# Kernel tuning notes

Hardware: AMD Instinct MI355X
Metric: run time of the kernel (lower is better)

## Reference

```python
import jax, jax.numpy as jnp
import numpy as np

IN_CH = 256
MED_CH = IN_CH // 2


def setup_inputs() -> dict:
    key = jax.random.key(0)
    ks = jax.random.split(key, 9)
    B, C, H, W = 16, IN_CH, 64, 64
    s = 1.0 / np.sqrt(C)
    sm = 1.0 / np.sqrt(MED_CH)
    return {
        "x": jax.random.normal(ks[0], (B, C, H, W), dtype=jnp.float32),
        "w_o": jax.random.normal(ks[1], (MED_CH, C), dtype=jnp.float32) * s,
        "b_o": jax.random.normal(ks[2], (MED_CH,), dtype=jnp.float32) * 0.01,
        "w_v": jax.random.normal(ks[3], (MED_CH, C), dtype=jnp.float32) * s,
        "b_v": jax.random.normal(ks[4], (MED_CH,), dtype=jnp.float32) * 0.01,
        "w_c": jax.random.normal(ks[5], (C, MED_CH), dtype=jnp.float32) * sm,
        "b_c": jax.random.normal(ks[6], (C,), dtype=jnp.float32) * 0.01,
        "gamma": jax.random.normal(ks[7], (1,), dtype=jnp.float32) * 0.1,
    }


def reference(x, w_o, b_o, w_v, b_v, w_c, b_c, gamma):
    B, C, H, W = x.shape
    N = H * W
    xf = x.reshape(B, C, N)  # [B,C,N]
    # 1x1 convs == per-pixel linear projections
    o = jnp.einsum("mc,bcn->bmn", w_o, xf) + b_o[None, :, None]   # [B,M,N]
    v = jnp.einsum("mc,bcn->bmn", w_v, xf) + b_v[None, :, None]   # [B,M,N]
    x_o = o.transpose(0, 2, 1)                                     # [B,N,M]
    x_v = jax.nn.softmax(v, axis=-1)                               # softmax over N
    # NOTE: original code reuses conv_v for the 's' branch (conv_s unused)
    x_s = jax.nn.softmax(v.transpose(0, 2, 1), axis=-1)            # [B,N,M], softmax over M
    A = jnp.einsum("bmn,bnk->bmk", x_v, x_s)                       # [B,M,M]
    Bt = jnp.einsum("bnm,bmk->bnk", x_o, A).transpose(0, 2, 1)     # [B,M,N]
    out = jax.nn.relu(jnp.einsum("cm,bmn->bcn", w_c, Bt) + b_c[None, :, None])
    result = gamma[0] * out.reshape(B, C, H, W) + x
    return result
```

## Files before the change

### kernel.cpp

```cpp
#include <hip/hip_runtime.h>
#include <math.h>

constexpr int Bn = 16;
constexpr int Cn = 256;
constexpr int Mn = 128;
constexpr int Nn = 4096;

typedef short bf16x8 __attribute__((ext_vector_type(8)));
typedef float f32x4 __attribute__((ext_vector_type(4)));
typedef unsigned short us8 __attribute__((ext_vector_type(8)));
typedef unsigned short us4 __attribute__((ext_vector_type(4)));

static __device__ __forceinline__ unsigned short f2bf(float f) {
  union { float f; unsigned int u; } c{f};
  unsigned int u = c.u;
  u += 0x7FFFu + ((u >> 16) & 1u);
  return (unsigned short)(u >> 16);
}

__global__ __launch_bounds__(256) void k_prep_w(
    const float* __restrict__ w_o, const float* __restrict__ w_v,
    unsigned short* __restrict__ Wst, float* __restrict__ rs) {
  int idx = blockIdx.x * 256 + threadIdx.x;
  if (idx < Bn * Mn) rs[idx] = 0.f;
  int row = idx >> 6;
  int c4 = (idx & 63) * 4;
  const float* src = (row < Mn) ? &w_o[(size_t)row * Cn + c4]
                                : &w_v[(size_t)(row - Mn) * Cn + c4];
  float4 f = *(const float4*)src;
  us4 g = {f2bf(f.x), f2bf(f.y), f2bf(f.z), f2bf(f.w)};
  *(us4*)&Wst[(size_t)row * Cn + c4] = g;
}

__global__ __launch_bounds__(256) void k_prep_x(
    const float* __restrict__ x, unsigned short* __restrict__ xT) {
  const int b = blockIdx.z;
  const int c0 = blockIdx.y * 128;
  const int n0 = blockIdx.x * 64;
  const int t = threadIdx.x;
  const int n4 = (t & 15) * 4;
  const int c8 = c0 + (t >> 4) * 8;
  const float* xb = x + ((size_t)b * Cn + c8) * Nn + n0 + n4;
  float4 r[8];
#pragma unroll
  for (int i = 0; i < 8; ++i) r[i] = *(const float4*)&xb[(size_t)i * Nn];
  unsigned short* dst = xT + ((size_t)b * Nn + n0 + n4) * Cn + c8;
#pragma unroll
  for (int j = 0; j < 4; ++j) {
    us8 g;
#pragma unroll
    for (int i = 0; i < 8; ++i) g[i] = f2bf(((const float*)&r[i])[j]);
    *(us8*)&dst[(size_t)j * Cn] = g;
  }
}

__global__ __launch_bounds__(256) void k_proj_mfma(
    const unsigned short* __restrict__ Wst,
    const unsigned short* __restrict__ xT,
    const float* __restrict__ b_o, const float* __restrict__ b_v,
    unsigned short* __restrict__ oT, float* __restrict__ Ap,
    float* __restrict__ rs) {
  __shared__ us8 pool[16 * 128 * 2];
  __shared__ float cs_lds[4][128];
  unsigned short* ldsA = (unsigned short*)pool;
  unsigned short* ldsB = (unsigned short*)pool + 8 * 128 * 8;
  const int b = blockIdx.z;
  const int mt = blockIdx.y;
  const int nt = blockIdx.x;
  const int t = threadIdx.x;
  const int wave = t >> 6, lane = t & 63;
  const int quad = lane >> 4, l16 = lane & 15;
  const int wm = (wave & 1) * 64, wn = (wave >> 1) * 64;
  f32x4 acc[4][4] = {};
  const unsigned short* Wb = Wst + (size_t)mt * 128 * Cn;
  const unsigned short* xb = xT + ((size_t)b * Nn + nt * 128) * Cn;

  for (int k0 = 0; k0 < Cn; k0 += 64) {
#pragma unroll
    for (int p = 0; p < 4; ++p) {
      int s = p * 256 + t;
      int g = s >> 7, row = s & 127;
      *(uint4*)&ldsA[(size_t)s * 8] = *(const uint4*)&Wb[(size_t)row * Cn + k0 + g * 8];
      *(uint4*)&ldsB[(size_t)s * 8] = *(const uint4*)&xb[(size_t)row * Cn + k0 + g * 8];
    }
    __syncthreads();
#pragma unroll
    for (int s = 0; s < 2; ++s) {
      bf16x8 af[4], bfr[4];
#pragma unroll
      for (int i = 0; i < 4; ++i)
        af[i] = *(const bf16x8*)&ldsA[(size_t)((s * 4 + quad) * 128 + wm + i * 16 + l16) * 8];
#pragma unroll
      for (int j = 0; j < 4; ++j)
        bfr[j] = *(const bf16x8*)&ldsB[(size_t)((s * 4 + quad) * 128 + wn + j * 16 + l16) * 8];
      if (mt) {
#pragma unroll
        for (int i = 0; i < 4; ++i)
#pragma unroll
          for (int j = 0; j < 4; ++j)
            acc[i][j] = __builtin_amdgcn_mfma_f32_16x16x32_bf16(af[i], bfr[j], acc[i][j], 0, 0, 0);
      } else {
#pragma unroll
        for (int i = 0; i < 4; ++i)
#pragma unroll
          for (int j = 0; j < 4; ++j)
            acc[i][j] = __builtin_amdgcn_mfma_f32_16x16x32_bf16(bfr[i], af[j], acc[i][j], 0, 0, 0);
      }
    }
    __syncthreads();
  }

  if (!mt) {
    float bo_j[4];
#pragma unroll
    for (int j = 0; j < 4; ++j) bo_j[j] = b_o[wm + j * 16 + l16];
#pragma unroll
    for (int i = 0; i < 4; ++i) {
#pragma unroll
      for (int r = 0; r < 4; ++r) {
        int n = nt * 128 + wn + i * 16 + quad * 4 + r;
        unsigned short* row = &oT[((size_t)b * Nn + n) * Mn];
#pragma unroll
        for (int j = 0; j < 4; ++j)
          row[wm + j * 16 + l16] = f2bf(acc[i][j][r] + bo_j[j]);
      }
    }
    return;
  }

#pragma unroll
  for (int i = 0; i < 4; ++i) {
#pragma unroll
    for (int r = 0; r < 4; ++r) {
      float bi = b_v[wm + i * 16 + quad * 4 + r];
#pragma unroll
      for (int j = 0; j < 4; ++j)
        acc[i][j][r] = __expf(acc[i][j][r] + bi);
    }
  }

#pragma unroll
  for (int i = 0; i < 4; ++i) {
#pragma unroll
    for (int r = 0; r < 4; ++r) {
      float s = acc[i][0][r] + acc[i][1][r] + acc[i][2][r] + acc[i][3][r];
      s += __shfl_xor(s, 1); s += __shfl_xor(s, 2);
      s += __shfl_xor(s, 4); s += __shfl_xor(s, 8);
      if (l16 == 0)
        atomicAdd(&rs[b * Mn + wm + i * 16 + quad * 4 + r], s);
    }
  }

  float csj[4];
#pragma unroll
  for (int j = 0; j < 4; ++j) {
    float c = 0.f;
#pragma unroll
    for (int i = 0; i < 4; ++i)
#pragma unroll
      for (int r = 0; r < 4; ++r) c += acc[i][j][r];
    c += __shfl_xor(c, 16);
    c += __shfl_xor(c, 32);
    csj[j] = c;
  }
  if (quad == 0) {
#pragma unroll
    for (int j = 0; j < 4; ++j) cs_lds[wave][wn + j * 16 + l16] = csj[j];
  }
  __syncthreads();

  const int cbase = (wave >> 1) * 2;
  float rinv[4];
#pragma unroll
  for (int j = 0; j < 4; ++j) {
    int nl = wn + j * 16 + l16;
    rinv[j] = rsqrtf(cs_lds[cbase][nl] + cs_lds[cbase + 1][nl]);
  }

  unsigned short* Hs = (unsigned short*)pool;
  unsigned short* Ls = Hs + 16 * 128 * 8;
#pragma unroll
  for (int i = 0; i < 4; ++i) {
#pragma unroll
    for (int r = 0; r < 4; ++r) {
      int m = wm + i * 16 + quad * 4 + r;
#pragma unroll
      for (int j = 0; j < 4; ++j) {
        int nl = wn + j * 16 + l16;
        float u = acc[i][j][r] * rinv[j];
        unsigned short h = f2bf(u);
        union { unsigned int q; float f; } hf{(unsigned int)h << 16};
        int idx = ((nl >> 3) * 128 + (m ^ (nl >> 3))) * 8 + (nl & 7);
        Hs[idx] = h;
        Ls[idx] = f2bf(u - hf.f);
      }
    }
  }
  __syncthreads();

  const bf16x8* Hv = (const bf16x8*)pool;
  const bf16x8* Lv = Hv + 16 * 128;
#pragma unroll
  for (int i = 0; i < 4; ++i)
#pragma unroll
    for (int j = 0; j < 4; ++j) acc[i][j] = (f32x4){0.f, 0.f, 0.f, 0.f};
#pragma unroll
  for (int s = 0; s < 4; ++s) {
    int g = s * 4 + quad;
    bf16x8 hA[4], lA[4], hB[4], lB[4];
#pragma unroll
    for (int i = 0; i < 4; ++i) {
      int mi = wm + i * 16 + l16;
      int ki = wn + i * 16 + l16;
      hA[i] = Hv[g * 128 + (mi ^ g)];
      lA[i] = Lv[g * 128 + (mi ^ g)];
      hB[i] = Hv[g * 128 + (ki ^ g)];
      lB[i] = Lv[g * 128 + (ki ^ g)];
    }
#pragma unroll
    for (int i = 0; i < 4; ++i)
#pragma unroll
      for (int j = 0; j < 4; ++j) {
        acc[i][j] = __builtin_amdgcn_mfma_f32_16x16x32_bf16(hA[i], hB[j], acc[i][j], 0, 0, 0);
        acc[i][j] = __builtin_amdgcn_mfma_f32_16x16x32_bf16(hA[i], lB[j], acc[i][j], 0, 0, 0);
        acc[i][j] = __builtin_amdgcn_mfma_f32_16x16x32_bf16(lA[i], hB[j], acc[i][j], 0, 0, 0);
      }
  }

  float* Apb = Ap + ((size_t)nt * Bn + b) * (Mn * Mn);
#pragma unroll
  for (int i = 0; i < 4; ++i) {
#pragma unroll
    for (int r = 0; r < 4; ++r) {
      int m = wm + i * 16 + quad * 4 + r;
      float* row = &Apb[(size_t)m * Mn];
#pragma unroll
      for (int j = 0; j < 4; ++j)
        row[wn + j * 16 + l16] = acc[i][j][r];
    }
  }
}

__global__ __launch_bounds__(256) void k_reduceA(
    const float* __restrict__ Ap, const float* __restrict__ rs,
    float* __restrict__ A, int S) {
  int tid = blockIdx.x * 256 + threadIdx.x;
  int idx4 = tid * 4;
  int b = idx4 / (Mn * Mn);
  int off = idx4 - b * (Mn * Mn);
  float4 s = {0.f, 0.f, 0.f, 0.f};
  for (int s0 = 0; s0 < S; ++s0) {
    float4 p = *(const float4*)&Ap[((size_t)s0 * Bn + b) * (Mn * Mn) + off];
    s.x += p.x; s.y += p.y; s.z += p.z; s.w += p.w;
  }
  float sc = 1.0f / rs[b * Mn + (off >> 7)];
  s.x *= sc; s.y *= sc; s.z *= sc; s.w *= sc;
  *(float4*)&A[idx4] = s;
}

__global__ __launch_bounds__(256) void k_w2(
    const float* __restrict__ w_c, const float* __restrict__ A,
    unsigned short* __restrict__ W2bf) {
  __shared__ float As[64][68];
  __shared__ float wcs[64][68];
  const int b = blockIdx.z;
  const int m0 = blockIdx.x * 64;
  const int c0 = blockIdx.y * 64;
  const int t = threadIdx.x;
  const int tc = (t >> 4) * 4, tmm = (t & 15) * 4;
  float acc[4][4] = {};
  for (int k0 = 0; k0 < Mn; k0 += 64) {
    int r = t >> 2;
    int k4 = (t & 3) * 4;
#pragma unroll
    for (int p = 0; p < 4; ++p) {
      int k = k4 + p * 16;
      float4 a4 = *(const float4*)&A[((size_t)(b * Mn + m0 + r)) * Mn + k0 + k];
      As[k + 0][r] = a4.x; As[k + 1][r] = a4.y; As[k + 2][r] = a4.z; As[k + 3][r] = a4.w;
      float4 w4 = *(const float4*)&w_c[(size_t)(c0 + r) * Mn + k0 + k];
      wcs[k + 0][r] = w4.x; wcs[k + 1][r] = w4.y; wcs[k + 2][r] = w4.z; wcs[k + 3][r] = w4.w;
    }
    __syncthreads();
#pragma unroll
    for (int kk = 0; kk < 64; ++kk) {
      float4 w4 = *(const float4*)&wcs[kk][tc];
      float4 a4 = *(const float4*)&As[kk][tmm];
      float w[4] = {w4.x, w4.y, w4.z, w4.w};
      float a[4] = {a4.x, a4.y, a4.z, a4.w};
#pragma unroll
      for (int i = 0; i < 4; ++i)
#pragma unroll
        for (int jj = 0; jj < 4; ++jj) acc[i][jj] = fmaf(w[i], a[jj], acc[i][jj]);
    }
    __syncthreads();
  }
#pragma unroll
  for (int i = 0; i < 4; ++i) {
    us4 g4 = {f2bf(acc[i][0]), f2bf(acc[i][1]), f2bf(acc[i][2]), f2bf(acc[i][3])};
    *(us4*)&W2bf[((size_t)(b * Cn + c0 + tc + i)) * Mn + m0 + tmm] = g4;
  }
}

__global__ __launch_bounds__(256) void k_final_mfma(
    const unsigned short* __restrict__ W2bf, const unsigned short* __restrict__ oT,
    const float* __restrict__ x, const float* __restrict__ b_c,
    const float* __restrict__ gamma, float* __restrict__ out) {
  __shared__ us8 ldsA[128 * 16];
  __shared__ us8 ldsB[128 * 16];
  const int b = blockIdx.z;
  const int c_t = blockIdx.y * 128;
  const int n_t = blockIdx.x * 128;
  const int t = threadIdx.x;
  const int wave = t >> 6, lane = t & 63;
  const int quad = lane >> 4, l16 = lane & 15;
  const int wc = (wave & 1) * 64, wn = (wave >> 1) * 64;
  const unsigned short* W2b = W2bf + ((size_t)b * Cn + c_t) * Mn;
  const unsigned short* oTb = oT + ((size_t)b * Nn + n_t) * Mn;

#pragma unroll
  for (int p = 0; p < 8; ++p) {
    int s = p * 256 + t;
    int row = s >> 4, g = s & 15;
    int slot = row * 16 + (g ^ (row & 15));
    ldsA[slot] = *(const us8*)&W2b[(size_t)row * Mn + g * 8];
    ldsB[slot] = *(const us8*)&oTb[(size_t)row * Mn + g * 8];
  }
  __syncthreads();

  f32x4 acc[4][4] = {};
#pragma unroll
  for (int s = 0; s < 4; ++s) {
    int gq = s * 4 + quad;
    int xo = gq ^ l16;
    bf16x8 af[4], bfr[4];
#pragma unroll
    for (int i = 0; i < 4; ++i)
      af[i] = *(const bf16x8*)&ldsA[(wc + i * 16 + l16) * 16 + xo];
#pragma unroll
    for (int j = 0; j < 4; ++j)
      bfr[j] = *(const bf16x8*)&ldsB[(wn + j * 16 + l16) * 16 + xo];
#pragma unroll
    for (int i = 0; i < 4; ++i)
#pragma unroll
      for (int j = 0; j < 4; ++j)
        acc[i][j] = __builtin_amdgcn_mfma_f32_16x16x32_bf16(af[i], bfr[j], acc[i][j], 0, 0, 0);
  }

  float g = gamma[0];
#pragma unroll
  for (int i = 0; i < 4; ++i) {
#pragma unroll
    for (int r = 0; r < 4; ++r) {
      int c = c_t + wc + i * 16 + quad * 4 + r;
      float bias = b_c[c];
      const float* xr = &x[((size_t)b * Cn + c) * Nn + n_t];
      float* orow = &out[((size_t)b * Cn + c) * Nn + n_t];
#pragma unroll
      for (int j = 0; j < 4; ++j) {
        int n = wn + j * 16 + l16;
        orow[n] = g * fmaxf(acc[i][j][r] + bias, 0.f) + xr[n];
      }
    }
  }
}

extern "C" void kernel_launch(void* const* d_in, const int* in_sizes, int n_in,
                              void* d_out, int out_size, void* d_ws, size_t ws_size,
                              hipStream_t stream) {
  const float* x   = (const float*)d_in[0];
  const float* w_o = (const float*)d_in[1];
  const float* b_o = (const float*)d_in[2];
  const float* w_v = (const float*)d_in[3];
  const float* b_v = (const float*)d_in[4];
  const float* w_c = (const float*)d_in[5];
  const float* b_c = (const float*)d_in[6];
  const float* gm  = (const float*)d_in[7];

  constexpr int S = Nn / 128;
  float* ws = (float*)d_ws;
  float* rs = ws;
  float* A  = rs + Bn * Mn;
  float* Ap = A + (size_t)Bn * Mn * Mn;
  unsigned short* oT   = (unsigned short*)(Ap + (size_t)S * Bn * Mn * Mn);
  unsigned short* W2bf = oT + (size_t)Bn * Nn * Mn;
  unsigned short* xT   = W2bf + (size_t)Bn * Cn * Mn;
  unsigned short* Wst  = xT + (size_t)Bn * Nn * Cn;

  k_prep_w<<<dim3(Cn * Cn / 1024), 256, 0, stream>>>(w_o, w_v, Wst, rs);
  k_prep_x<<<dim3(Nn / 64, 2, Bn), 256, 0, stream>>>(x, xT);
  k_proj_mfma<<<dim3(Nn / 128, 2, Bn), 256, 0, stream>>>(Wst, xT, b_o, b_v, oT, Ap, rs);
  k_reduceA<<<dim3(Bn * Mn * Mn / 1024), 256, 0, stream>>>(Ap, rs, A, S);
  k_w2<<<dim3(Mn / 64, Cn / 64, Bn), 256, 0, stream>>>(w_c, A, W2bf);
  k_final_mfma<<<dim3(Nn / 128, Cn / 128, Bn), 256, 0, stream>>>(W2bf, oT, x, b_c, gm, (float*)d_out);
}
```

Before: 232.7 us.

## Split Gram computation into separate kernel with atomic accumulation and async LDS loads

The per-tile Gram product is moved out of the projection kernel into a new k_gram kernel. It reads packed hi/lo bf16 values from global memory and accumulates A with atomicAdd, which removes the partial-A buffer and the reduction kernel. The 1/rs scaling moves into k_w2, and A is zeroed in k_prep_w. The projection kernel now uses global_load_lds for the W tile, register prefetch of the next x tile, and launch bounds of 3 blocks per SM. This adds a global round trip for the packed U values and makes the fp32 summation order nondeterministic.

```diff
diff --git a/kernel.cpp b/kernel.cpp
--- a/kernel.cpp
+++ b/kernel.cpp
@@ -18,11 +18,21 @@
   return (unsigned short)(u >> 16);
 }
 
+static __device__ __forceinline__ void gload_lds16(const void* g, void* l) {
+  __builtin_amdgcn_global_load_lds(
+      (const __attribute__((address_space(1))) unsigned int*)g,
+      (__attribute__((address_space(3))) unsigned int*)l, 16, 0, 0);
+}
+
 __global__ __launch_bounds__(256) void k_prep_w(
     const float* __restrict__ w_o, const float* __restrict__ w_v,
-    unsigned short* __restrict__ Wst, float* __restrict__ rs) {
+    unsigned short* __restrict__ Wst, float* __restrict__ rs,
+    float* __restrict__ A) {
   int idx = blockIdx.x * 256 + threadIdx.x;
   if (idx < Bn * Mn) rs[idx] = 0.f;
+  float4 z = {0.f, 0.f, 0.f, 0.f};
+  float4* Az = (float4*)A + (size_t)idx * 4;
+  Az[0] = z; Az[1] = z; Az[2] = z; Az[3] = z;
   int row = idx >> 6;
   int c4 = (idx & 63) * 4;
   const float* src = (row < Mn) ? &w_o[(size_t)row * Cn + c4]
@@ -54,16 +64,15 @@
   }
 }
 
-__global__ __launch_bounds__(256) void k_proj_mfma(
+__global__ __launch_bounds__(256, 3) void k_proj_mfma(
     const unsigned short* __restrict__ Wst,
     const unsigned short* __restrict__ xT,
     const float* __restrict__ b_o, const float* __restrict__ b_v,
-    unsigned short* __restrict__ oT, float* __restrict__ Ap,
+    unsigned short* __restrict__ oT, unsigned int* __restrict__ Upk,
     float* __restrict__ rs) {
-  __shared__ us8 pool[16 * 128 * 2];
+  __shared__ unsigned short ldsA[8 * 128 * 8];
+  __shared__ unsigned short ldsB[8 * 128 * 8];
   __shared__ float cs_lds[4][128];
-  unsigned short* ldsA = (unsigned short*)pool;
-  unsigned short* ldsB = (unsigned short*)pool + 8 * 128 * 8;
   const int b = blockIdx.z;
   const int mt = blockIdx.y;
   const int nt = blockIdx.x;
@@ -74,16 +83,28 @@
   f32x4 acc[4][4] = {};
   const unsigned short* Wb = Wst + (size_t)mt * 128 * Cn;
   const unsigned short* xb = xT + ((size_t)b * Nn + nt * 128) * Cn;
+  const int rowS = t & 127;
+  const int gS = t >> 7;
+
+  uint4 rB[4];
+#pragma unroll
+  for (int p = 0; p < 4; ++p)
+    rB[p] = *(const uint4*)&xb[(size_t)rowS * Cn + (p * 2 + gS) * 8];
 
   for (int k0 = 0; k0 < Cn; k0 += 64) {
 #pragma unroll
     for (int p = 0; p < 4; ++p) {
       int s = p * 256 + t;
-      int g = s >> 7, row = s & 127;
-      *(uint4*)&ldsA[(size_t)s * 8] = *(const uint4*)&Wb[(size_t)row * Cn + k0 + g * 8];
-      *(uint4*)&ldsB[(size_t)s * 8] = *(const uint4*)&xb[(size_t)row * Cn + k0 + g * 8];
-    }
-    __syncthreads();
+      *(uint4*)&ldsB[(size_t)s * 8] = rB[p];
+      gload_lds16(&Wb[(size_t)rowS * Cn + k0 + (p * 2 + gS) * 8],
+                  &ldsA[(size_t)s * 8]);
+    }
+    __syncthreads();
+    if (k0 + 64 < Cn) {
+#pragma unroll
+      for (int p = 0; p < 4; ++p)
+        rB[p] = *(const uint4*)&xb[(size_t)rowS * Cn + k0 + 64 + (p * 2 + gS) * 8];
+    }
 #pragma unroll
     for (int s = 0; s < 2; ++s) {
       bf16x8 af[4], bfr[4];
@@ -177,8 +198,7 @@
     rinv[j] = rsqrtf(cs_lds[cbase][nl] + cs_lds[cbase + 1][nl]);
   }
 
-  unsigned short* Hs = (unsigned short*)pool;
-  unsigned short* Ls = Hs + 16 * 128 * 8;
+  unsigned int* Ub = Upk + (size_t)(b * 32 + nt) * (16 * 128 * 8);
 #pragma unroll
   for (int i = 0; i < 4; ++i) {
 #pragma unroll
@@ -190,77 +210,86 @@
         float u = acc[i][j][r] * rinv[j];
         unsigned short h = f2bf(u);
         union { unsigned int q; float f; } hf{(unsigned int)h << 16};
-        int idx = ((nl >> 3) * 128 + (m ^ (nl >> 3))) * 8 + (nl & 7);
-        Hs[idx] = h;
-        Ls[idx] = f2bf(u - hf.f);
-      }
-    }
-  }
-  __syncthreads();
-
-  const bf16x8* Hv = (const bf16x8*)pool;
-  const bf16x8* Lv = Hv + 16 * 128;
-#pragma unroll
-  for (int i = 0; i < 4; ++i)
-#pragma unroll
-    for (int j = 0; j < 4; ++j) acc[i][j] = (f32x4){0.f, 0.f, 0.f, 0.f};
-#pragma unroll
-  for (int s = 0; s < 4; ++s) {
-    int g = s * 4 + quad;
-    bf16x8 hA[4], lA[4], hB[4], lB[4];
-#pragma unroll
-    for (int i = 0; i < 4; ++i) {
-      int mi = wm + i * 16 + l16;
-      int ki = wn + i * 16 + l16;
-      hA[i] = Hv[g * 128 + (mi ^ g)];
-      lA[i] = Lv[g * 128 + (mi ^ g)];
-      hB[i] = Hv[g * 128 + (ki ^ g)];
-      lB[i] = Lv[g * 128 + (ki ^ g)];
-    }
-#pragma unroll
-    for (int i = 0; i < 4; ++i)
-#pragma unroll
-      for (int j = 0; j < 4; ++j) {
-        acc[i][j] = __builtin_amdgcn_mfma_f32_16x16x32_bf16(hA[i], hB[j], acc[i][j], 0, 0, 0);
-        acc[i][j] = __builtin_amdgcn_mfma_f32_16x16x32_bf16(hA[i], lB[j], acc[i][j], 0, 0, 0);
-        acc[i][j] = __builtin_amdgcn_mfma_f32_16x16x32_bf16(lA[i], hB[j], acc[i][j], 0, 0, 0);
-      }
-  }
-
-  float* Apb = Ap + ((size_t)nt * Bn + b) * (Mn * Mn);
+        unsigned short lo = f2bf(u - hf.f);
+        Ub[((size_t)(nl >> 3) * 128 + m) * 8 + (nl & 7)] =
+            ((unsigned int)h << 16) | lo;
+      }
+    }
+  }
+}
+
+__global__ __launch_bounds__(256, 3) void k_gram(
+    const unsigned int* __restrict__ Upk, float* __restrict__ A) {
+  __shared__ us8 Hs[8 * 128];
+  __shared__ us8 Ls[8 * 128];
+  const int b = blockIdx.y;
+  const int nt = blockIdx.x;
+  const int t = threadIdx.x;
+  const int wave = t >> 6, lane = t & 63;
+  const int quad = lane >> 4, l16 = lane & 15;
+  const int wm = (wave & 1) * 64, wk = (wave >> 1) * 64;
+  const unsigned int* Ub = Upk + (size_t)(b * 32 + nt) * (16 * 128 * 8);
+  f32x4 acc[4][4] = {};
+
+  for (int p = 0; p < 2; ++p) {
+#pragma unroll
+    for (int p4 = 0; p4 < 4; ++p4) {
+      int q = p4 * 256 + t;
+      const unsigned int* src = &Ub[((size_t)(p * 8 + (q >> 7)) * 128 + (q & 127)) * 8];
+      uint4 w0 = *(const uint4*)src;
+      uint4 w1 = *(const uint4*)(src + 4);
+      unsigned int ww[8] = {w0.x, w0.y, w0.z, w0.w, w1.x, w1.y, w1.z, w1.w};
+      us8 h8, l8;
+#pragma unroll
+      for (int e = 0; e < 8; ++e) {
+        h8[e] = (unsigned short)(ww[e] >> 16);
+        l8[e] = (unsigned short)(ww[e] & 0xffffu);
+      }
+      Hs[q] = h8;
+      Ls[q] = l8;
+    }
+    __syncthreads();
+#pragma unroll
+    for (int s = 0; s < 2; ++s) {
+      int g = s * 4 + quad;
+      bf16x8 hA[4], lA[4], hB[4], lB[4];
+#pragma unroll
+      for (int i = 0; i < 4; ++i) {
+        int mi = wm + i * 16 + l16;
+        int ki = wk + i * 16 + l16;
+        hA[i] = *(const bf16x8*)&Hs[g * 128 + mi];
+        lA[i] = *(const bf16x8*)&Ls[g * 128 + mi];
+        hB[i] = *(const bf16x8*)&Hs[g * 128 + ki];
+        lB[i] = *(const bf16x8*)&Ls[g * 128 + ki];
+      }
+#pragma unroll
+      for (int i = 0; i < 4; ++i)
+#pragma unroll
+        for (int j = 0; j < 4; ++j) {
+          acc[i][j] = __builtin_amdgcn_mfma_f32_16x16x32_bf16(hA[i], hB[j], acc[i][j], 0, 0, 0);
+          acc[i][j] = __builtin_amdgcn_mfma_f32_16x16x32_bf16(hA[i], lB[j], acc[i][j], 0, 0, 0);
+          acc[i][j] = __builtin_amdgcn_mfma_f32_16x16x32_bf16(lA[i], hB[j], acc[i][j], 0, 0, 0);
+        }
+    }
+    __syncthreads();
+  }
+
+  float* Ab = A + (size_t)b * Mn * Mn;
 #pragma unroll
   for (int i = 0; i < 4; ++i) {
 #pragma unroll
     for (int r = 0; r < 4; ++r) {
       int m = wm + i * 16 + quad * 4 + r;
-      float* row = &Apb[(size_t)m * Mn];
 #pragma unroll
       for (int j = 0; j < 4; ++j)
-        row[wn + j * 16 + l16] = acc[i][j][r];
-    }
-  }
-}
-
-__global__ __launch_bounds__(256) void k_reduceA(
-    const float* __restrict__ Ap, const float* __restrict__ rs,
-    float* __restrict__ A, int S) {
-  int tid = blockIdx.x * 256 + threadIdx.x;
-  int idx4 = tid * 4;
-  int b = idx4 / (Mn * Mn);
-  int off = idx4 - b * (Mn * Mn);
-  float4 s = {0.f, 0.f, 0.f, 0.f};
-  for (int s0 = 0; s0 < S; ++s0) {
-    float4 p = *(const float4*)&Ap[((size_t)s0 * Bn + b) * (Mn * Mn) + off];
-    s.x += p.x; s.y += p.y; s.z += p.z; s.w += p.w;
-  }
-  float sc = 1.0f / rs[b * Mn + (off >> 7)];
-  s.x *= sc; s.y *= sc; s.z *= sc; s.w *= sc;
-  *(float4*)&A[idx4] = s;
+        atomicAdd(&Ab[(size_t)m * Mn + wk + j * 16 + l16], acc[i][j][r]);
+    }
+  }
 }
 
 __global__ __launch_bounds__(256) void k_w2(
     const float* __restrict__ w_c, const float* __restrict__ A,
-    unsigned short* __restrict__ W2bf) {
+    const float* __restrict__ rs, unsigned short* __restrict__ W2bf) {
   __shared__ float As[64][68];
   __shared__ float wcs[64][68];
   const int b = blockIdx.z;
@@ -268,15 +297,17 @@
   const int c0 = blockIdx.y * 64;
   const int t = threadIdx.x;
   const int tc = (t >> 4) * 4, tmm = (t & 15) * 4;
+  const int r = t >> 2;
+  const int k4 = (t & 3) * 4;
+  const float irs = 1.0f / rs[b * Mn + m0 + r];
   float acc[4][4] = {};
   for (int k0 = 0; k0 < Mn; k0 += 64) {
-    int r = t >> 2;
-    int k4 = (t & 3) * 4;
 #pragma unroll
     for (int p = 0; p < 4; ++p) {
       int k = k4 + p * 16;
       float4 a4 = *(const float4*)&A[((size_t)(b * Mn + m0 + r)) * Mn + k0 + k];
-      As[k + 0][r] = a4.x; As[k + 1][r] = a4.y; As[k + 2][r] = a4.z; As[k + 3][r] = a4.w;
+      As[k + 0][r] = a4.x * irs; As[k + 1][r] = a4.y * irs;
+      As[k + 2][r] = a4.z * irs; As[k + 3][r] = a4.w * irs;
       float4 w4 = *(const float4*)&w_c[(size_t)(c0 + r) * Mn + k0 + k];
       wcs[k + 0][r] = w4.x; wcs[k + 1][r] = w4.y; wcs[k + 2][r] = w4.z; wcs[k + 3][r] = w4.w;
     }
@@ -376,20 +407,19 @@
   const float* b_c = (const float*)d_in[6];
   const float* gm  = (const float*)d_in[7];
 
-  constexpr int S = Nn / 128;
   float* ws = (float*)d_ws;
   float* rs = ws;
   float* A  = rs + Bn * Mn;
-  float* Ap = A + (size_t)Bn * Mn * Mn;
-  unsigned short* oT   = (unsigned short*)(Ap + (size_t)S * Bn * Mn * Mn);
+  unsigned int* Upk = (unsigned int*)(A + (size_t)Bn * Mn * Mn);
+  unsigned short* oT   = (unsigned short*)(Upk + (size_t)Bn * Nn * Mn);
   unsigned short* W2bf = oT + (size_t)Bn * Nn * Mn;
   unsigned short* xT   = W2bf + (size_t)Bn * Cn * Mn;
   unsigned short* Wst  = xT + (size_t)Bn * Nn * Cn;
 
-  k_prep_w<<<dim3(Cn * Cn / 1024), 256, 0, stream>>>(w_o, w_v, Wst, rs);
+  k_prep_w<<<dim3(Cn * Cn / 1024), 256, 0, stream>>>(w_o, w_v, Wst, rs, A);
   k_prep_x<<<dim3(Nn / 64, 2, Bn), 256, 0, stream>>>(x, xT);
-  k_proj_mfma<<<dim3(Nn / 128, 2, Bn), 256, 0, stream>>>(Wst, xT, b_o, b_v, oT, Ap, rs);
-  k_reduceA<<<dim3(Bn * Mn * Mn / 1024), 256, 0, stream>>>(Ap, rs, A, S);
-  k_w2<<<dim3(Mn / 64, Cn / 64, Bn), 256, 0, stream>>>(w_c, A, W2bf);
+  k_proj_mfma<<<dim3(Nn / 128, 2, Bn), 256, 0, stream>>>(Wst, xT, b_o, b_v, oT, Upk, rs);
+  k_gram<<<dim3(Nn / 128, Bn), 256, 0, stream>>>(Upk, A);
+  k_w2<<<dim3(Mn / 64, Cn / 64, Bn), 256, 0, stream>>>(w_c, A, rs, W2bf);
   k_final_mfma<<<dim3(Nn / 128, Cn / 128, Bn), 256, 0, stream>>>(W2bf, oT, x, b_c, gm, (float*)d_out);
 }
```

Result: slower. 266.9 us (+14.7%).

## Fold o-projection into output weights and drop the oT intermediate

Applied to the files above, without the earlier changes.

Reassociates the math so that w_c·A·w_o is precomputed per batch as a CxC matrix (WW) with a combined bias (bb). The final GEMM then reads xT directly with K=256, so the o-projection GEMM and the oT write and read are no longer needed. The v-projection kernel now uses global_load_lds for the weights and register prefetch of the next x tile. The cost is a small extra k_ww kernel and doubled K in the final GEMM, plus an extra bf16 rounding of the fused weights.

```diff
diff --git a/kernel.cpp b/kernel.cpp
--- a/kernel.cpp
+++ b/kernel.cpp
@@ -18,18 +18,33 @@
   return (unsigned short)(u >> 16);
 }
 
+static __device__ __forceinline__ void gload_lds16(const void* g, void* l) {
+  __builtin_amdgcn_global_load_lds(
+      (const __attribute__((address_space(1))) unsigned int*)g,
+      (__attribute__((address_space(3))) unsigned int*)l, 16, 0, 0);
+}
+
 __global__ __launch_bounds__(256) void k_prep_w(
     const float* __restrict__ w_o, const float* __restrict__ w_v,
-    unsigned short* __restrict__ Wst, float* __restrict__ rs) {
+    unsigned short* __restrict__ Wv, unsigned short* __restrict__ woT,
+    float* __restrict__ rs) {
   int idx = blockIdx.x * 256 + threadIdx.x;
   if (idx < Bn * Mn) rs[idx] = 0.f;
-  int row = idx >> 6;
-  int c4 = (idx & 63) * 4;
-  const float* src = (row < Mn) ? &w_o[(size_t)row * Cn + c4]
-                                : &w_v[(size_t)(row - Mn) * Cn + c4];
-  float4 f = *(const float4*)src;
-  us4 g = {f2bf(f.x), f2bf(f.y), f2bf(f.z), f2bf(f.w)};
-  *(us4*)&Wst[(size_t)row * Cn + c4] = g;
+  if (idx < 8192) {
+    int row = idx >> 6;
+    int c4 = (idx & 63) * 4;
+    float4 f = *(const float4*)&w_v[(size_t)row * Cn + c4];
+    us4 g = {f2bf(f.x), f2bf(f.y), f2bf(f.z), f2bf(f.w)};
+    *(us4*)&Wv[(size_t)row * Cn + c4] = g;
+  } else {
+    int j = idx - 8192;
+    int cp = j >> 5;
+    int m4 = (j & 31) * 4;
+    us4 g;
+#pragma unroll
+    for (int e = 0; e < 4; ++e) g[e] = f2bf(w_o[(size_t)(m4 + e) * Cn + cp]);
+    *(us4*)&woT[(size_t)cp * Mn + m4] = g;
+  }
 }
 
 __global__ __launch_bounds__(256) void k_prep_x(
@@ -54,36 +69,45 @@
   }
 }
 
-__global__ __launch_bounds__(256) void k_proj_mfma(
-    const unsigned short* __restrict__ Wst,
+__global__ __launch_bounds__(256) void k_proj_v(
+    const unsigned short* __restrict__ Wv,
     const unsigned short* __restrict__ xT,
-    const float* __restrict__ b_o, const float* __restrict__ b_v,
-    unsigned short* __restrict__ oT, float* __restrict__ Ap,
-    float* __restrict__ rs) {
+    const float* __restrict__ b_v,
+    float* __restrict__ Ap, float* __restrict__ rs) {
   __shared__ us8 pool[16 * 128 * 2];
   __shared__ float cs_lds[4][128];
   unsigned short* ldsA = (unsigned short*)pool;
   unsigned short* ldsB = (unsigned short*)pool + 8 * 128 * 8;
-  const int b = blockIdx.z;
-  const int mt = blockIdx.y;
+  const int b = blockIdx.y;
   const int nt = blockIdx.x;
   const int t = threadIdx.x;
   const int wave = t >> 6, lane = t & 63;
   const int quad = lane >> 4, l16 = lane & 15;
   const int wm = (wave & 1) * 64, wn = (wave >> 1) * 64;
   f32x4 acc[4][4] = {};
-  const unsigned short* Wb = Wst + (size_t)mt * 128 * Cn;
   const unsigned short* xb = xT + ((size_t)b * Nn + nt * 128) * Cn;
+  const int rowS = t & 127;
+  const int gS = t >> 7;
+
+  uint4 rB[4];
+#pragma unroll
+  for (int p = 0; p < 4; ++p)
+    rB[p] = *(const uint4*)&xb[(size_t)rowS * Cn + (p * 2 + gS) * 8];
 
   for (int k0 = 0; k0 < Cn; k0 += 64) {
 #pragma unroll
     for (int p = 0; p < 4; ++p) {
       int s = p * 256 + t;
-      int g = s >> 7, row = s & 127;
-      *(uint4*)&ldsA[(size_t)s * 8] = *(const uint4*)&Wb[(size_t)row * Cn + k0 + g * 8];
-      *(uint4*)&ldsB[(size_t)s * 8] = *(const uint4*)&xb[(size_t)row * Cn + k0 + g * 8];
-    }
-    __syncthreads();
+      *(uint4*)&ldsB[(size_t)s * 8] = rB[p];
+      gload_lds16(&Wv[(size_t)rowS * Cn + k0 + (p * 2 + gS) * 8],
+                  &ldsA[(size_t)s * 8]);
+    }
+    __syncthreads();
+    if (k0 + 64 < Cn) {
+#pragma unroll
+      for (int p = 0; p < 4; ++p)
+        rB[p] = *(const uint4*)&xb[(size_t)rowS * Cn + k0 + 64 + (p * 2 + gS) * 8];
+    }
 #pragma unroll
     for (int s = 0; s < 2; ++s) {
       bf16x8 af[4], bfr[4];
@@ -93,39 +117,13 @@
 #pragma unroll
       for (int j = 0; j < 4; ++j)
         bfr[j] = *(const bf16x8*)&ldsB[(size_t)((s * 4 + quad) * 128 + wn + j * 16 + l16) * 8];
-      if (mt) {
-#pragma unroll
-        for (int i = 0; i < 4; ++i)
-#pragma unroll
-          for (int j = 0; j < 4; ++j)
-            acc[i][j] = __builtin_amdgcn_mfma_f32_16x16x32_bf16(af[i], bfr[j], acc[i][j], 0, 0, 0);
-      } else {
-#pragma unroll
-        for (int i = 0; i < 4; ++i)
-#pragma unroll
-          for (int j = 0; j < 4; ++j)
-            acc[i][j] = __builtin_amdgcn_mfma_f32_16x16x32_bf16(bfr[i], af[j], acc[i][j], 0, 0, 0);
-      }
-    }
-    __syncthreads();
-  }
-
-  if (!mt) {
-    float bo_j[4];
-#pragma unroll
-    for (int j = 0; j < 4; ++j) bo_j[j] = b_o[wm + j * 16 + l16];
-#pragma unroll
-    for (int i = 0; i < 4; ++i) {
-#pragma unroll
-      for (int r = 0; r < 4; ++r) {
-        int n = nt * 128 + wn + i * 16 + quad * 4 + r;
-        unsigned short* row = &oT[((size_t)b * Nn + n) * Mn];
+#pragma unroll
+      for (int i = 0; i < 4; ++i)
 #pragma unroll
         for (int j = 0; j < 4; ++j)
-          row[wm + j * 16 + l16] = f2bf(acc[i][j][r] + bo_j[j]);
-      }
-    }
-    return;
+          acc[i][j] = __builtin_amdgcn_mfma_f32_16x16x32_bf16(af[i], bfr[j], acc[i][j], 0, 0, 0);
+    }
+    __syncthreads();
   }
 
 #pragma unroll
@@ -301,9 +299,83 @@
   }
 }
 
+__global__ __launch_bounds__(256) void k_ww(
+    const unsigned short* __restrict__ W2bf, const unsigned short* __restrict__ woT,
+    const float* __restrict__ b_o, const float* __restrict__ b_c,
+    unsigned short* __restrict__ WW, float* __restrict__ bb) {
+  __shared__ us8 ldsA[128 * 16];
+  __shared__ us8 ldsB[128 * 16];
+  __shared__ float bo_lds[128];
+  const int b = blockIdx.z;
+  const int c_t = blockIdx.y * 128;
+  const int cp_t = blockIdx.x * 128;
+  const int t = threadIdx.x;
+  const int wave = t >> 6, lane = t & 63;
+  const int quad = lane >> 4, l16 = lane & 15;
+  const int wc = (wave & 1) * 64, wp = (wave >> 1) * 64;
+  const unsigned short* W2b = W2bf + ((size_t)b * Cn + c_t) * Mn;
+  const unsigned short* woB = woT + (size_t)cp_t * Mn;
+
+#pragma unroll
+  for (int p = 0; p < 8; ++p) {
+    int s = p * 256 + t;
+    int row = s >> 4, g = s & 15;
+    int slot = row * 16 + (g ^ (row & 15));
+    ldsA[slot] = *(const us8*)&W2b[(size_t)row * Mn + g * 8];
+    ldsB[slot] = *(const us8*)&woB[(size_t)row * Mn + g * 8];
+  }
+  if (blockIdx.x == 0 && t < 128) bo_lds[t] = b_o[t];
+  __syncthreads();
+
+  f32x4 acc[4][4] = {};
+#pragma unroll
+  for (int s = 0; s < 4; ++s) {
+    int gq = s * 4 + quad;
+    int xo = gq ^ l16;
+    bf16x8 af[4], bfr[4];
+#pragma unroll
+    for (int i = 0; i < 4; ++i)
+      af[i] = *(const bf16x8*)&ldsA[(wc + i * 16 + l16) * 16 + xo];
+#pragma unroll
+    for (int j = 0; j < 4; ++j)
+      bfr[j] = *(const bf16x8*)&ldsB[(wp + j * 16 + l16) * 16 + xo];
+#pragma unroll
+    for (int i = 0; i < 4; ++i)
+#pragma unroll
+      for (int j = 0; j < 4; ++j)
+        acc[i][j] = __builtin_amdgcn_mfma_f32_16x16x32_bf16(af[i], bfr[j], acc[i][j], 0, 0, 0);
+  }
+
+#pragma unroll
+  for (int i = 0; i < 4; ++i) {
+#pragma unroll
+    for (int r = 0; r < 4; ++r) {
+      int c = c_t + wc + i * 16 + quad * 4 + r;
+      unsigned short* row = &WW[((size_t)b * Cn + c) * Cn + cp_t];
+#pragma unroll
+      for (int j = 0; j < 4; ++j)
+        row[wp + j * 16 + l16] = f2bf(acc[i][j][r]);
+    }
+  }
+
+  if (blockIdx.x == 0 && t < 128) {
+    float s = 0.f;
+#pragma unroll
+    for (int g = 0; g < 16; ++g) {
+      us8 h = ldsA[t * 16 + (g ^ (t & 15))];
+#pragma unroll
+      for (int e = 0; e < 8; ++e) {
+        union { unsigned int u; float f; } cv{(unsigned int)h[e] << 16};
+        s = fmaf(cv.f, bo_lds[g * 8 + e], s);
+      }
+    }
+    bb[b * Cn + c_t + t] = s + b_c[c_t + t];
+  }
+}
+
 __global__ __launch_bounds__(256) void k_final_mfma(
-    const unsigned short* __restrict__ W2bf, const unsigned short* __restrict__ oT,
-    const float* __restrict__ x, const float* __restrict__ b_c,
+    const unsigned short* __restrict__ WW, const unsigned short* __restrict__ xT,
+    const float* __restrict__ x, const float* __restrict__ bb,
     const float* __restrict__ gamma, float* __restrict__ out) {
   __shared__ us8 ldsA[128 * 16];
   __shared__ us8 ldsB[128 * 16];
@@ -314,36 +386,38 @@
   const int wave = t >> 6, lane = t & 63;
   const int quad = lane >> 4, l16 = lane & 15;
   const int wc = (wave & 1) * 64, wn = (wave >> 1) * 64;
-  const unsigned short* W2b = W2bf + ((size_t)b * Cn + c_t) * Mn;
-  const unsigned short* oTb = oT + ((size_t)b * Nn + n_t) * Mn;
-
-#pragma unroll
-  for (int p = 0; p < 8; ++p) {
-    int s = p * 256 + t;
-    int row = s >> 4, g = s & 15;
-    int slot = row * 16 + (g ^ (row & 15));
-    ldsA[slot] = *(const us8*)&W2b[(size_t)row * Mn + g * 8];
-    ldsB[slot] = *(const us8*)&oTb[(size_t)row * Mn + g * 8];
-  }
-  __syncthreads();
+  const unsigned short* WWb = WW + ((size_t)b * Cn + c_t) * Cn;
+  const unsigned short* xTb = xT + ((size_t)b * Nn + n_t) * Cn;
 
   f32x4 acc[4][4] = {};
-#pragma unroll
-  for (int s = 0; s < 4; ++s) {
-    int gq = s * 4 + quad;
-    int xo = gq ^ l16;
-    bf16x8 af[4], bfr[4];
-#pragma unroll
-    for (int i = 0; i < 4; ++i)
-      af[i] = *(const bf16x8*)&ldsA[(wc + i * 16 + l16) * 16 + xo];
-#pragma unroll
-    for (int j = 0; j < 4; ++j)
-      bfr[j] = *(const bf16x8*)&ldsB[(wn + j * 16 + l16) * 16 + xo];
-#pragma unroll
-    for (int i = 0; i < 4; ++i)
-#pragma unroll
-      for (int j = 0; j < 4; ++j)
-        acc[i][j] = __builtin_amdgcn_mfma_f32_16x16x32_bf16(af[i], bfr[j], acc[i][j], 0, 0, 0);
+  for (int k0 = 0; k0 < Cn; k0 += 128) {
+#pragma unroll
+    for (int p = 0; p < 8; ++p) {
+      int s = p * 256 + t;
+      int row = s >> 4, g = s & 15;
+      int slot = row * 16 + (g ^ (row & 15));
+      ldsA[slot] = *(const us8*)&WWb[(size_t)row * Cn + k0 + g * 8];
+      ldsB[slot] = *(const us8*)&xTb[(size_t)row * Cn + k0 + g * 8];
+    }
+    __syncthreads();
+#pragma unroll
+    for (int s = 0; s < 4; ++s) {
+      int gq = s * 4 + quad;
+      int xo = gq ^ l16;
+      bf16x8 af[4], bfr[4];
+#pragma unroll
+      for (int i = 0; i < 4; ++i)
+        af[i] = *(const bf16x8*)&ldsA[(wc + i * 16 + l16) * 16 + xo];
+#pragma unroll
+      for (int j = 0; j < 4; ++j)
+        bfr[j] = *(const bf16x8*)&ldsB[(wn + j * 16 + l16) * 16 + xo];
+#pragma unroll
+      for (int i = 0; i < 4; ++i)
+#pragma unroll
+        for (int j = 0; j < 4; ++j)
+          acc[i][j] = __builtin_amdgcn_mfma_f32_16x16x32_bf16(af[i], bfr[j], acc[i][j], 0, 0, 0);
+    }
+    __syncthreads();
   }
 
   float g = gamma[0];
@@ -352,7 +426,7 @@
 #pragma unroll
     for (int r = 0; r < 4; ++r) {
       int c = c_t + wc + i * 16 + quad * 4 + r;
-      float bias = b_c[c];
+      float bias = bb[b * Cn + c];
       const float* xr = &x[((size_t)b * Cn + c) * Nn + n_t];
       float* orow = &out[((size_t)b * Cn + c) * Nn + n_t];
 #pragma unroll
@@ -379,17 +453,20 @@
   constexpr int S = Nn / 128;
   float* ws = (float*)d_ws;
   float* rs = ws;
-  float* A  = rs + Bn * Mn;
+  float* bb = rs + Bn * Mn;
+  float* A  = bb + Bn * Cn;
   float* Ap = A + (size_t)Bn * Mn * Mn;
-  unsigned short* oT   = (unsigned short*)(Ap + (size_t)S * Bn * Mn * Mn);
-  unsigned short* W2bf = oT + (size_t)Bn * Nn * Mn;
+  unsigned short* WW   = (unsigned short*)(Ap + (size_t)S * Bn * Mn * Mn);
+  unsigned short* W2bf = WW + (size_t)Bn * Cn * Cn;
   unsigned short* xT   = W2bf + (size_t)Bn * Cn * Mn;
-  unsigned short* Wst  = xT + (size_t)Bn * Nn * Cn;
-
-  k_prep_w<<<dim3(Cn * Cn / 1024), 256, 0, stream>>>(w_o, w_v, Wst, rs);
+  unsigned short* Wv   = xT + (size_t)Bn * Nn * Cn;
+  unsigned short* woT  = Wv + (size_t)Mn * Cn;
+
+  k_prep_w<<<dim3(64), 256, 0, stream>>>(w_o, w_v, Wv, woT, rs);
   k_prep_x<<<dim3(Nn / 64, 2, Bn), 256, 0, stream>>>(x, xT);
-  k_proj_mfma<<<dim3(Nn / 128, 2, Bn), 256, 0, stream>>>(Wst, xT, b_o, b_v, oT, Ap, rs);
+  k_proj_v<<<dim3(Nn / 128, Bn), 256, 0, stream>>>(Wv, xT, b_v, Ap, rs);
   k_reduceA<<<dim3(Bn * Mn * Mn / 1024), 256, 0, stream>>>(Ap, rs, A, S);
   k_w2<<<dim3(Mn / 64, Cn / 64, Bn), 256, 0, stream>>>(w_c, A, W2bf);
-  k_final_mfma<<<dim3(Nn / 128, Cn / 128, Bn), 256, 0, stream>>>(W2bf, oT, x, b_c, gm, (float*)d_out);
-}
+  k_ww<<<dim3(2, 2, Bn), 256, 0, stream>>>(W2bf, woT, b_o, b_c, WW, bb);
+  k_final_mfma<<<dim3(Nn / 128, Cn / 128, Bn), 256, 0, stream>>>(WW, xT, x, bb, gm, (float*)d_out);
+}
```

Result: faster. 210.2 us (-9.7%).
